# Optimization experiments

Hardware: AMD Instinct MI355X
Metric: run time of the kernel (lower is better)

Reference implementation:

```python
import jax, jax.numpy as jnp
import numpy as np

L, R = -0.1, 1.1          # HardKuma stretched support
MAX_REL = 11              # max relative distance
CLAMP_LO, CLAMP_HI = 0.01, 100.0


def setup_inputs() -> dict:
    key = jax.random.key(0)
    ks = jax.random.split(key, 12)
    B, T, Din, Dout = 4, 2048, 512, 256
    s_in = 0.02
    return {
        "q": jax.random.normal(ks[0], (B, T, Din), jnp.float32),
        "k": jax.random.normal(ks[1], (B, T, Din), jnp.float32),
        "Wa1": jax.random.normal(ks[2], (Din, Dout), jnp.float32) * s_in,
        "ba1": jnp.zeros((Dout,), jnp.float32),
        "Wa2": jax.random.normal(ks[3], (Dout, Dout), jnp.float32) * s_in,
        "ba2": jnp.zeros((Dout,), jnp.float32),
        "Wb1": jax.random.normal(ks[4], (Din, Dout), jnp.float32) * s_in,
        "bb1": jnp.zeros((Dout,), jnp.float32),
        "Wb2": jax.random.normal(ks[5], (Dout, Dout), jnp.float32) * s_in,
        "bb2": jnp.zeros((Dout,), jnp.float32),
        "dist_emb": jax.random.normal(ks[6], (2 * MAX_REL + 1,), jnp.float32) * 0.02,
    }


def _mlp(x, W1, b1, W2, b2):
    # Sequential(Linear, ReLU, Dropout, Linear, ReLU, Dropout) in eval mode
    h = jax.nn.relu(x @ W1 + b1)
    return jax.nn.relu(h @ W2 + b2)


def _rel_dists(T, dist_emb):
    i = jnp.arange(T)
    rel = jnp.clip(i[None, :] - i[:, None], -MAX_REL, MAX_REL) + MAX_REL  # [T,T] ints in [0,22]
    return dist_emb[rel]  # [T,T]


def _kuma_cdf(t, a, b):
    # F(t; a, b) = 1 - (1 - t^a)^b, t is a positive Python-float constant
    return 1.0 - jnp.power(1.0 - jnp.power(t, a), b)


def _kuma_mean(a, b):
    # E[X] = b * Beta(1 + 1/a, b)
    g = 1.0 + 1.0 / a
    return b * jnp.exp(jax.scipy.special.gammaln(g) + jax.scipy.special.gammaln(b)
                       - jax.scipy.special.gammaln(g + b))


def reference(q, k, Wa1, ba1, Wa2, ba2, Wb1, bb1, Wb2, bb2, dist_emb):
    T = q.shape[1]
    q_a = _mlp(q, Wa1, ba1, Wa2, ba2)
    k_a = _mlp(k, Wa1, ba1, Wa2, ba2)
    q_b = _mlp(q, Wb1, bb1, Wb2, bb2)
    k_b = _mlp(k, Wb1, bb1, Wb2, bb2)

    a = jnp.einsum("btd,bsd->bts", q_a, k_a)  # [B,T,T]
    b = jnp.einsum("btd,bsd->bts", q_b, k_b)

    rd = _rel_dists(T, dist_emb)[None]  # [1,T,T]
    a = a + rd
    b = b + rd

    a = jnp.clip(jax.nn.softplus(a), CLAMP_LO, CLAMP_HI)
    b = jnp.clip(jax.nn.softplus(b), CLAMP_LO, CLAMP_HI)

    # HardKuma deterministic (eval) attention
    t0 = (0.0 - L) / (R - L)  # stretched coord of 0
    t1 = (1.0 - L) / (R - L)  # stretched coord of 1
    p0 = _kuma_cdf(t0, a, b)          # P(h = 0)
    p1 = 1.0 - _kuma_cdf(t1, a, b)    # P(h = 1)
    pc = 1.0 - p0 - p1                # continuous mass

    mean = jnp.clip(L + (R - L) * _kuma_mean(a, b), 0.0, 1.0)
    zero_one = jnp.where(p0 > p1, 0.0, 1.0)
    att = jnp.where(pc < 0.5, zero_one, mean)
    return att
```

## Files before the change

### kernel.cpp

```cpp
#include <hip/hip_runtime.h>
#include <hip/hip_bf16.h>
#include <math.h>

typedef __hip_bfloat16 bf16;
typedef short bf16x8 __attribute__((ext_vector_type(8)));
typedef float f32x4 __attribute__((ext_vector_type(4)));
typedef float f32x2 __attribute__((ext_vector_type(2)));

union alignas(16) Pack8 { bf16 h[8]; bf16x8 v; };

#define EXP2F(x) __builtin_amdgcn_exp2f(x)
#define LOG2F(x) __builtin_amdgcn_logf(x)
#define RCPF(x)  __builtin_amdgcn_rcpf(x)

#define TAB_N   64
#define TAB_LO  (-0.35f)
#define TAB_HI  (1.25f)
#define TAB_STRIDE 65

__device__ __forceinline__ float stirl2s(float z) {
    float iz = 1.f / z;
    return (z - 0.5f) * LOG2F(z) - 1.44269504f * z + 1.32574806f
         + iz * (0.12022651f - 0.00400749f * iz * iz);
}
__device__ __forceinline__ float sp4s(float x) {
    return (x * (x + 1.f)) * ((x + 2.f) * (x + 3.f));
}
__device__ float mean_f32(float sa, float sb) {
    float lw = LOG2F(1.f + EXP2F(sa * 1.44269504f));
    float lv = LOG2F(1.f + EXP2F(sb * 1.44269504f));
    lw = fminf(fmaxf(lw, 0.01442695f), 144.269504f);
    lv = fminf(fmaxf(lv, 0.01442695f), 144.269504f);
    float b = 0.69314718f * lv;
    float g = 1.44269504f / lw + 1.f;
    float gb = g + b;
    float lb2 = stirl2s(g + 4.f) + stirl2s(b + 4.f) - stirl2s(gb + 4.f)
              + LOG2F(sp4s(gb) / (sp4s(g) * sp4s(b)));
    float mean = fmaf(1.2f * b, EXP2F(lb2), -0.1f);
    return fminf(fmaxf(mean, 0.f), 1.f);
}

__global__ void prep_weights(const float* __restrict__ Wa1, const float* __restrict__ Wa2,
                             const float* __restrict__ Wb1, const float* __restrict__ Wb2,
                             bf16* __restrict__ oa1, bf16* __restrict__ oa2,
                             bf16* __restrict__ ob1, bf16* __restrict__ ob2,
                             float* __restrict__ tab) {
    if (blockIdx.x >= 1536) {
        int idx = (blockIdx.x - 1536) * 256 + threadIdx.x;
        if (idx >= TAB_N * TAB_N) return;
        int ia = idx >> 6, ib = idx & 63;
        const float step = (TAB_HI - TAB_LO) / (TAB_N - 1);
        float sa  = TAB_LO + ia * step;
        float sb  = TAB_LO + ib * step;
        int ib1 = ib < TAB_N - 1 ? ib + 1 : ib;
        float sb1 = TAB_LO + ib1 * step;
        tab[(ia * TAB_STRIDE + ib) * 2]     = mean_f32(sa, sb);
        tab[(ia * TAB_STRIDE + ib) * 2 + 1] = mean_f32(sa, sb1);
        return;
    }
    int idx = blockIdx.x * 256 + threadIdx.x;
    if (idx < 131072) {
        int n = idx >> 9, k = idx & 511;
        oa1[idx] = __float2bfloat16(Wa1[k * 256 + n]);
    } else if (idx < 196608) {
        int i = idx - 131072; int n = i >> 8, k = i & 255;
        oa2[i] = __float2bfloat16(Wa2[k * 256 + n]);
    } else if (idx < 327680) {
        int i = idx - 196608; int n = i >> 9, k = i & 511;
        ob1[i] = __float2bfloat16(Wb1[k * 256 + n]);
    } else {
        int i = idx - 327680; int n = i >> 8, k = i & 255;
        ob2[i] = __float2bfloat16(Wb2[k * 256 + n]);
    }
}

__global__ __launch_bounds__(512, 4)
void mlp_fused(const float* __restrict__ q, const float* __restrict__ k,
               const bf16* __restrict__ Wa1t, const bf16* __restrict__ Wa2t,
               const bf16* __restrict__ Wb1t, const bf16* __restrict__ Wb2t,
               bf16* __restrict__ qa, bf16* __restrict__ ka,
               bf16* __restrict__ qb, bf16* __restrict__ kb) {
    const int z = blockIdx.z;
    const float* X  = (z & 1) ? k : q;
    const bf16*  W1 = (z >> 1) ? Wb1t : Wa1t;
    const bf16*  W2 = (z >> 1) ? Wb2t : Wa2t;
    bf16* Y = (z == 0) ? qa : (z == 1) ? ka : (z == 2) ? qb : kb;
    const int m0 = blockIdx.x * 64;

    __shared__ alignas(16) char smem[54272];
    short* lB = (short*)smem;
    short* lH = (short*)(smem + 20480);
    short* lA = (short*)(smem + 20480);

    const int tid  = threadIdx.x;
    const int wave = tid >> 6, lane = tid & 63;
    const int wn = wave * 32;
    const int quad = lane >> 4, r16 = lane & 15;

    {
        f32x4 acc[4][2] = {};
        for (int kk = 0; kk < 512; kk += 32) {
            if (tid < 256) {
                int r = tid >> 2, c = (tid & 3) * 8;
                const float* p = X + (size_t)(m0 + r) * 512 + kk + c;
                Pack8 u;
#pragma unroll
                for (int j = 0; j < 8; j++) u.h[j] = __float2bfloat16(p[j]);
                *(bf16x8*)&lA[r * 40 + c] = u.v;
            }
            for (int i = tid; i < 1024; i += 512) {
                int r = i >> 2, c = (i & 3) * 8;
                *(bf16x8*)&lB[r * 40 + c] =
                    *(const bf16x8*)(W1 + (size_t)r * 512 + kk + c);
            }
            __syncthreads();
            bf16x8 af[4], bfr[2];
#pragma unroll
            for (int f = 0; f < 4; f++)
                af[f] = *(const bf16x8*)&lA[(f * 16 + r16) * 40 + quad * 8];
#pragma unroll
            for (int f = 0; f < 2; f++)
                bfr[f] = *(const bf16x8*)&lB[(wn + f * 16 + r16) * 40 + quad * 8];
#pragma unroll
            for (int i = 0; i < 4; i++)
#pragma unroll
                for (int j = 0; j < 2; j++)
                    acc[i][j] = __builtin_amdgcn_mfma_f32_16x16x32_bf16(
                        af[i], bfr[j], acc[i][j], 0, 0, 0);
            __syncthreads();
        }
#pragma unroll
        for (int i = 0; i < 4; i++)
#pragma unroll
            for (int j = 0; j < 2; j++)
#pragma unroll
                for (int r = 0; r < 4; r++) {
                    float v = acc[i][j][r];
                    v = v > 0.f ? v : 0.f;
                    ((bf16*)lH)[(i * 16 + quad * 4 + r) * 264 + wn + j * 16 + r16] =
                        __float2bfloat16(v);
                }
    }
    __syncthreads();

    f32x4 acc2[4][2] = {};
    for (int kk = 0; kk < 256; kk += 32) {
        for (int i = tid; i < 1024; i += 512) {
            int r = i >> 2, c = (i & 3) * 8;
            *(bf16x8*)&lB[r * 40 + c] =
                *(const bf16x8*)(W2 + (size_t)r * 256 + kk + c);
        }
        __syncthreads();
        bf16x8 af[4], bfr[2];
#pragma unroll
        for (int f = 0; f < 4; f++)
            af[f] = *(const bf16x8*)&lH[(f * 16 + r16) * 264 + kk + quad * 8];
#pragma unroll
        for (int f = 0; f < 2; f++)
            bfr[f] = *(const bf16x8*)&lB[(wn + f * 16 + r16) * 40 + quad * 8];
#pragma unroll
        for (int i = 0; i < 4; i++)
#pragma unroll
            for (int j = 0; j < 2; j++)
                acc2[i][j] = __builtin_amdgcn_mfma_f32_16x16x32_bf16(
                    af[i], bfr[j], acc2[i][j], 0, 0, 0);
        __syncthreads();
    }

#pragma unroll
    for (int i = 0; i < 4; i++) {
        int rbase = m0 + i * 16 + quad * 4;
#pragma unroll
        for (int j = 0; j < 2; j++) {
            int col = wn + j * 16 + r16;
#pragma unroll
            for (int r = 0; r < 4; r++) {
                float v = acc2[i][j][r];
                v = v > 0.f ? v : 0.f;
                Y[(size_t)(rbase + r) * 256 + col] = __float2bfloat16(v);
            }
        }
    }
}

__device__ __forceinline__ f32x2 vexp2(f32x2 x) {
    f32x2 r; r.x = EXP2F(x.x); r.y = EXP2F(x.y); return r;
}
__device__ __forceinline__ f32x2 vlog2(f32x2 x) {
    f32x2 r; r.x = LOG2F(x.x); r.y = LOG2F(x.y); return r;
}
__device__ __forceinline__ f32x2 vrcp(f32x2 x) {
    f32x2 r; r.x = RCPF(x.x); r.y = RCPF(x.y); return r;
}
__device__ __forceinline__ f32x2 vclamp(f32x2 x, float lo, float hi) {
    f32x2 r;
    r.x = fminf(fmaxf(x.x, lo), hi);
    r.y = fminf(fmaxf(x.y, lo), hi);
    return r;
}

__device__ __noinline__ f32x2 hardkuma_slow(f32x2 la, f32x2 lb) {
    const float LOG2E = 1.44269504f;
    f32x2 lw = vlog2(1.f + vexp2(la * LOG2E));
    f32x2 lv = vlog2(1.f + vexp2(lb * LOG2E));
    lw = vclamp(lw, 0.01442695f, 144.269504f);
    lv = vclamp(lv, 0.01442695f, 144.269504f);
    f32x2 b = 0.69314718f * lv;

    f32x2 t0a = vexp2(-2.48490665f * lw);
    f32x2 t1a = vexp2(-0.08701138f * lw);
    f32x2 q0 = vexp2(b * vlog2(1.f - t0a));
    f32x2 p1 = vexp2(b * vlog2(1.f - t1a));
    f32x2 pc = q0 - p1;
    f32x2 p0 = 1.f - q0;

    f32x2 g  = 1.44269504f * vrcp(lw) + 1.f;
    f32x2 gb = g + b;
    f32x2 g2 = g + 2.f, b2 = b + 2.f, gb2 = gb + 2.f;

    f32x2 s = (g + 1.5f) * vlog2(g2) + (b + 1.5f) * vlog2(b2)
            - (gb + 1.5f) * vlog2(gb2);

    const float C1 = 0.12022459f;
    const float C2 = -0.00400749f;
    f32x2 pg  = g2 * b2;
    f32x2 rr3 = vrcp(pg * gb2);
    f32x2 ig  = rr3 * (b2 * gb2);
    f32x2 ib  = rr3 * (g2 * gb2);
    f32x2 igb = rr3 * pg;
    f32x2 corr = ig  * (C1 + C2 * (ig  * ig))
               + ib  * (C1 + C2 * (ib  * ib))
               - igb * (C1 + C2 * (igb * igb));
    s += corr - 1.55964202f;

    f32x2 ng = g * (g + 1.f), nb = b * (b + 1.f), ngb = gb * (gb + 1.f);
    s += vlog2(ngb * vrcp(ng * nb));

    f32x2 mean = (1.2f * b) * vexp2(s) - 0.1f;
    mean = vclamp(mean, 0.f, 1.f);

    f32x2 att;
    att.x = (pc.x < 0.5f) ? ((p0.x > p1.x) ? 0.f : 1.f) : mean.x;
    att.y = (pc.y < 0.5f) ? ((p0.y > p1.y) ? 0.f : 1.f) : mean.y;
    return att;
}

__global__ __launch_bounds__(512, 4)
void kuma_attn(const bf16* __restrict__ qa, const bf16* __restrict__ ka,
               const bf16* __restrict__ qb, const bf16* __restrict__ kb,
               const float* __restrict__ dist_emb, const float* __restrict__ tabg,
               float* __restrict__ out) {
    const int bidx = blockIdx.z;
    const int t0 = blockIdx.x * 128;
    const int s0 = blockIdx.y * 128;

    __shared__ alignas(16) char smem[41052];
    short* lQa = (short*)smem;
    short* lQb = (short*)(smem + 10240);
    short* lKa = (short*)(smem + 20480);
    short* lKb = (short*)(smem + 30720);
    float* sTab  = (float*)smem;
    float* sDist = (float*)(smem + 40960);

    const int tid = threadIdx.x;
    if (tid < 23) sDist[tid] = dist_emb[tid];

    const int wave = tid >> 6, lane = tid & 63;
    const int wm = (wave >> 2) * 64;
    const int wn = (wave & 3) * 32;
    const int quad = lane >> 4, r16 = lane & 15;
    const size_t base = (size_t)bidx * 2048 * 256;

    f32x4 accA[4][2] = {};
    f32x4 accB[4][2] = {};

    const int r0 = tid >> 2, c0 = (tid & 3) * 8;

    for (int kk = 0; kk < 256; kk += 32) {
        {
            size_t gq = base + (size_t)(t0 + r0) * 256 + kk + c0;
            size_t gk = base + (size_t)(s0 + r0) * 256 + kk + c0;
            *(bf16x8*)&lQa[r0 * 40 + c0] = *(const bf16x8*)(qa + gq);
            *(bf16x8*)&lQb[r0 * 40 + c0] = *(const bf16x8*)(qb + gq);
            *(bf16x8*)&lKa[r0 * 40 + c0] = *(const bf16x8*)(ka + gk);
            *(bf16x8*)&lKb[r0 * 40 + c0] = *(const bf16x8*)(kb + gk);
        }
        __syncthreads();
        bf16x8 aA[4], aB[4], bA[2], bB[2];
#pragma unroll
        for (int f = 0; f < 4; f++) {
            int ar = (wm + f * 16 + r16) * 40 + quad * 8;
            aA[f] = *(const bf16x8*)&lQa[ar];
            aB[f] = *(const bf16x8*)&lQb[ar];
        }
#pragma unroll
        for (int f = 0; f < 2; f++) {
            int br = (wn + f * 16 + r16) * 40 + quad * 8;
            bA[f] = *(const bf16x8*)&lKa[br];
            bB[f] = *(const bf16x8*)&lKb[br];
        }
#pragma unroll
        for (int i = 0; i < 4; i++)
#pragma unroll
            for (int j = 0; j < 2; j++) {
                accA[i][j] = __builtin_amdgcn_mfma_f32_16x16x32_bf16(
                    aA[i], bA[j], accA[i][j], 0, 0, 0);
                accB[i][j] = __builtin_amdgcn_mfma_f32_16x16x32_bf16(
                    aB[i], bB[j], accB[i][j], 0, 0, 0);
            }
        __syncthreads();
    }

    for (int i = tid; i < (TAB_N * TAB_STRIDE * 2) / 4; i += 512)
        ((f32x4*)sTab)[i] = ((const f32x4*)tabg)[i];
    __syncthreads();

    const float SCALE = (TAB_N - 1) / (TAB_HI - TAB_LO);
#pragma unroll
    for (int i = 0; i < 4; i++) {
#pragma unroll
        for (int j = 0; j < 2; j++) {
            int s = s0 + wn + j * 16 + r16;
#pragma unroll
            for (int rr = 0; rr < 2; rr++) {
                int t = t0 + wm + i * 16 + quad * 4 + rr * 2;
                int d0 = s - t;
                int d1 = d0 - 1;
                d0 = d0 < -11 ? -11 : (d0 > 11 ? 11 : d0);
                d1 = d1 < -11 ? -11 : (d1 > 11 ? 11 : d1);
                float rd0 = sDist[d0 + 11];
                float rd1 = sDist[d1 + 11];
                f32x2 la  = { accA[i][j][rr * 2] + rd0, accA[i][j][rr * 2 + 1] + rd1 };
                f32x2 lbv = { accB[i][j][rr * 2] + rd0, accB[i][j][rr * 2 + 1] + rd1 };

                float mn = fminf(fminf(la.x, la.y), fminf(lbv.x, lbv.y));
                float mx = fmaxf(fmaxf(la.x, la.y), fmaxf(lbv.x, lbv.y));

                f32x2 u = vclamp((la  - TAB_LO) * SCALE, 0.f, (float)(TAB_N - 1));
                f32x2 v = vclamp((lbv - TAB_LO) * SCALE, 0.f, (float)(TAB_N - 1));
                int ia0 = (int)u.x; ia0 = ia0 > TAB_N - 2 ? TAB_N - 2 : ia0;
                int ia1 = (int)u.y; ia1 = ia1 > TAB_N - 2 ? TAB_N - 2 : ia1;
                int ib0 = (int)v.x; ib0 = ib0 > TAB_N - 2 ? TAB_N - 2 : ib0;
                int ib1 = (int)v.y; ib1 = ib1 > TAB_N - 2 ? TAB_N - 2 : ib1;
                f32x2 fa = { u.x - (float)ia0, u.y - (float)ia1 };
                f32x2 fb = { v.x - (float)ib0, v.y - (float)ib1 };
                int o0 = (ia0 * TAB_STRIDE + ib0) * 2;
                int o1 = (ia1 * TAB_STRIDE + ib1) * 2;
                f32x2 e0r0 = *(const f32x2*)&sTab[o0];
                f32x2 e0r1 = *(const f32x2*)&sTab[o0 + TAB_STRIDE * 2];
                f32x2 e1r0 = *(const f32x2*)&sTab[o1];
                f32x2 e1r1 = *(const f32x2*)&sTab[o1 + TAB_STRIDE * 2];
                f32x2 m0 = { e0r0.x + fb.x * (e0r0.y - e0r0.x),
                             e1r0.x + fb.y * (e1r0.y - e1r0.x) };
                f32x2 m1 = { e0r1.x + fb.x * (e0r1.y - e0r1.x),
                             e1r1.x + fb.y * (e1r1.y - e1r1.x) };
                f32x2 att = m0 + fa * (m1 - m0);

                bool oob = (mn < TAB_LO) | (mx > TAB_HI);
                if (__builtin_expect(__any(oob), 0)) {
                    f32x2 ex = hardkuma_slow(la, lbv);
                    if (oob) att = ex;
                }

                out[((size_t)bidx * 2048 + t) * 2048 + s] = att.x;
                out[((size_t)bidx * 2048 + t + 1) * 2048 + s] = att.y;
            }
        }
    }
}

extern "C" void kernel_launch(void* const* d_in, const int* in_sizes, int n_in,
                              void* d_out, int out_size, void* d_ws, size_t ws_size,
                              hipStream_t stream) {
    const float* q    = (const float*)d_in[0];
    const float* k    = (const float*)d_in[1];
    const float* Wa1  = (const float*)d_in[2];
    const float* Wa2  = (const float*)d_in[4];
    const float* Wb1  = (const float*)d_in[6];
    const float* Wb2  = (const float*)d_in[8];
    const float* dist = (const float*)d_in[10];
    float* out = (float*)d_out;

    bf16* wsbf = (bf16*)d_ws;
    bf16* Wa1t = wsbf;
    bf16* Wa2t = Wa1t + 131072;
    bf16* Wb1t = Wa2t + 65536;
    bf16* Wb2t = Wb1t + 131072;
    bf16* qa   = Wb2t + 65536;
    bf16* ka   = qa + 2097152;
    bf16* qb   = ka + 2097152;
    bf16* kb   = qb + 2097152;
    bf16* tail = kb + 2097152;
    float* tabg = (float*)tail;

    prep_weights<<<1552, 256, 0, stream>>>(Wa1, Wa2, Wb1, Wb2,
                                           Wa1t, Wa2t, Wb1t, Wb2t, tabg);

    dim3 g1(128, 1, 4), blk512(512, 1, 1);
    mlp_fused<<<g1, blk512, 0, stream>>>(q, k, Wa1t, Wa2t, Wb1t, Wb2t,
                                         qa, ka, qb, kb);

    dim3 g2(16, 16, 4);
    kuma_attn<<<g2, blk512, 0, stream>>>(qa, ka, qb, kb, dist, tabg, out);
}
```

Measured before the change: 185.9 us.

## Use direct global-to-LDS loads and widen K tile to 64 in both GEMM kernels

Replaces register-staged global-to-shared copies of weights and Q/K projections with global_load_lds 16-byte direct loads, and doubles the K step per iteration from 32 to 64, which halves the number of barriers. The goal is to cut VGPR traffic and synchronisation overhead in the MLP and attention GEMM phases. The shared layouts lose their padding (row stride 64 instead of 40), which risks LDS bank conflicts on the MFMA fragment reads. LDS use per block also grows (up to about 66 KB), which may lower occupancy.

```diff
diff --git a/kernel.cpp b/kernel.cpp
--- a/kernel.cpp
+++ b/kernel.cpp
@@ -12,6 +12,12 @@
 #define EXP2F(x) __builtin_amdgcn_exp2f(x)
 #define LOG2F(x) __builtin_amdgcn_logf(x)
 #define RCPF(x)  __builtin_amdgcn_rcpf(x)
+
+__device__ __forceinline__ void gload16(const void* g, void* l) {
+    __builtin_amdgcn_global_load_lds(
+        (const __attribute__((address_space(1))) void*)g,
+        (__attribute__((address_space(3))) void*)l, 16, 0, 0);
+}
 
 #define TAB_N   64
 #define TAB_LO  (-0.35f)
@@ -87,46 +93,52 @@
     bf16* Y = (z == 0) ? qa : (z == 1) ? ka : (z == 2) ? qb : kb;
     const int m0 = blockIdx.x * 64;
 
-    __shared__ alignas(16) char smem[54272];
+    __shared__ alignas(16) char smem[66560];
     short* lB = (short*)smem;
-    short* lH = (short*)(smem + 20480);
-    short* lA = (short*)(smem + 20480);
+    short* lH = (short*)(smem + 32768);
+    short* lA = (short*)(smem + 32768);
 
     const int tid  = threadIdx.x;
     const int wave = tid >> 6, lane = tid & 63;
     const int wn = wave * 32;
     const int quad = lane >> 4, r16 = lane & 15;
+    const int srow = lane >> 3, scol = (lane & 7) * 8;
+    const int car = tid >> 3,  cac = (tid & 7) * 8;
 
     {
         f32x4 acc[4][2] = {};
-        for (int kk = 0; kk < 512; kk += 32) {
-            if (tid < 256) {
-                int r = tid >> 2, c = (tid & 3) * 8;
-                const float* p = X + (size_t)(m0 + r) * 512 + kk + c;
+        for (int kk = 0; kk < 512; kk += 64) {
+            {
+                const float* p = X + (size_t)(m0 + car) * 512 + kk + cac;
                 Pack8 u;
 #pragma unroll
                 for (int j = 0; j < 8; j++) u.h[j] = __float2bfloat16(p[j]);
-                *(bf16x8*)&lA[r * 40 + c] = u.v;
-            }
-            for (int i = tid; i < 1024; i += 512) {
-                int r = i >> 2, c = (i & 3) * 8;
-                *(bf16x8*)&lB[r * 40 + c] =
-                    *(const bf16x8*)(W1 + (size_t)r * 512 + kk + c);
+                *(bf16x8*)&lA[car * 64 + cac] = u.v;
+            }
+#pragma unroll
+            for (int j = 0; j < 4; j++) {
+                int row = wave * 32 + j * 8 + srow;
+                gload16(W1 + (size_t)row * 512 + kk + scol,
+                        lB + (wave * 32 + j * 8) * 64);
             }
             __syncthreads();
-            bf16x8 af[4], bfr[2];
-#pragma unroll
-            for (int f = 0; f < 4; f++)
-                af[f] = *(const bf16x8*)&lA[(f * 16 + r16) * 40 + quad * 8];
-#pragma unroll
-            for (int f = 0; f < 2; f++)
-                bfr[f] = *(const bf16x8*)&lB[(wn + f * 16 + r16) * 40 + quad * 8];
-#pragma unroll
-            for (int i = 0; i < 4; i++)
-#pragma unroll
-                for (int j = 0; j < 2; j++)
-                    acc[i][j] = __builtin_amdgcn_mfma_f32_16x16x32_bf16(
-                        af[i], bfr[j], acc[i][j], 0, 0, 0);
+#pragma unroll
+            for (int ks = 0; ks < 2; ks++) {
+                int co = ks * 32 + quad * 8;
+                bf16x8 af[4], bfr[2];
+#pragma unroll
+                for (int f = 0; f < 4; f++)
+                    af[f] = *(const bf16x8*)&lA[(f * 16 + r16) * 64 + co];
+#pragma unroll
+                for (int f = 0; f < 2; f++)
+                    bfr[f] = *(const bf16x8*)&lB[(wn + f * 16 + r16) * 64 + co];
+#pragma unroll
+                for (int i = 0; i < 4; i++)
+#pragma unroll
+                    for (int j = 0; j < 2; j++)
+                        acc[i][j] = __builtin_amdgcn_mfma_f32_16x16x32_bf16(
+                            af[i], bfr[j], acc[i][j], 0, 0, 0);
+            }
             __syncthreads();
         }
 #pragma unroll
@@ -144,26 +156,31 @@
     __syncthreads();
 
     f32x4 acc2[4][2] = {};
-    for (int kk = 0; kk < 256; kk += 32) {
-        for (int i = tid; i < 1024; i += 512) {
-            int r = i >> 2, c = (i & 3) * 8;
-            *(bf16x8*)&lB[r * 40 + c] =
-                *(const bf16x8*)(W2 + (size_t)r * 256 + kk + c);
+    for (int kk = 0; kk < 256; kk += 64) {
+#pragma unroll
+        for (int j = 0; j < 4; j++) {
+            int row = wave * 32 + j * 8 + srow;
+            gload16(W2 + (size_t)row * 256 + kk + scol,
+                    lB + (wave * 32 + j * 8) * 64);
         }
         __syncthreads();
-        bf16x8 af[4], bfr[2];
-#pragma unroll
-        for (int f = 0; f < 4; f++)
-            af[f] = *(const bf16x8*)&lH[(f * 16 + r16) * 264 + kk + quad * 8];
-#pragma unroll
-        for (int f = 0; f < 2; f++)
-            bfr[f] = *(const bf16x8*)&lB[(wn + f * 16 + r16) * 40 + quad * 8];
-#pragma unroll
-        for (int i = 0; i < 4; i++)
-#pragma unroll
-            for (int j = 0; j < 2; j++)
-                acc2[i][j] = __builtin_amdgcn_mfma_f32_16x16x32_bf16(
-                    af[i], bfr[j], acc2[i][j], 0, 0, 0);
+#pragma unroll
+        for (int ks = 0; ks < 2; ks++) {
+            int co = kk + ks * 32 + quad * 8;
+            bf16x8 af[4], bfr[2];
+#pragma unroll
+            for (int f = 0; f < 4; f++)
+                af[f] = *(const bf16x8*)&lH[(f * 16 + r16) * 264 + co];
+#pragma unroll
+            for (int f = 0; f < 2; f++)
+                bfr[f] = *(const bf16x8*)&lB[(wn + f * 16 + r16) * 64 + ks * 32 + quad * 8];
+#pragma unroll
+            for (int i = 0; i < 4; i++)
+#pragma unroll
+                for (int j = 0; j < 2; j++)
+                    acc2[i][j] = __builtin_amdgcn_mfma_f32_16x16x32_bf16(
+                        af[i], bfr[j], acc2[i][j], 0, 0, 0);
+        }
         __syncthreads();
     }
 
@@ -254,13 +271,13 @@
     const int t0 = blockIdx.x * 128;
     const int s0 = blockIdx.y * 128;
 
-    __shared__ alignas(16) char smem[41052];
+    __shared__ alignas(16) char smem[65628];
     short* lQa = (short*)smem;
-    short* lQb = (short*)(smem + 10240);
-    short* lKa = (short*)(smem + 20480);
-    short* lKb = (short*)(smem + 30720);
+    short* lQb = (short*)(smem + 16384);
+    short* lKa = (short*)(smem + 32768);
+    short* lKb = (short*)(smem + 49152);
     float* sTab  = (float*)smem;
-    float* sDist = (float*)(smem + 40960);
+    float* sDist = (float*)(smem + 65536);
 
     const int tid = threadIdx.x;
     if (tid < 23) sDist[tid] = dist_emb[tid];
@@ -271,43 +288,50 @@
     const int quad = lane >> 4, r16 = lane & 15;
     const size_t base = (size_t)bidx * 2048 * 256;
 
+    const int srow = lane >> 3, scol = (lane & 7) * 8;
+
     f32x4 accA[4][2] = {};
     f32x4 accB[4][2] = {};
 
-    const int r0 = tid >> 2, c0 = (tid & 3) * 8;
-
-    for (int kk = 0; kk < 256; kk += 32) {
-        {
-            size_t gq = base + (size_t)(t0 + r0) * 256 + kk + c0;
-            size_t gk = base + (size_t)(s0 + r0) * 256 + kk + c0;
-            *(bf16x8*)&lQa[r0 * 40 + c0] = *(const bf16x8*)(qa + gq);
-            *(bf16x8*)&lQb[r0 * 40 + c0] = *(const bf16x8*)(qb + gq);
-            *(bf16x8*)&lKa[r0 * 40 + c0] = *(const bf16x8*)(ka + gk);
-            *(bf16x8*)&lKb[r0 * 40 + c0] = *(const bf16x8*)(kb + gk);
+    for (int kk = 0; kk < 256; kk += 64) {
+#pragma unroll
+        for (int j = 0; j < 2; j++) {
+            int row = wave * 16 + j * 8 + srow;
+            size_t gq = base + (size_t)(t0 + row) * 256 + kk + scol;
+            size_t gk = base + (size_t)(s0 + row) * 256 + kk + scol;
+            int ld = (wave * 16 + j * 8) * 64;
+            gload16(qa + gq, lQa + ld);
+            gload16(qb + gq, lQb + ld);
+            gload16(ka + gk, lKa + ld);
+            gload16(kb + gk, lKb + ld);
         }
         __syncthreads();
-        bf16x8 aA[4], aB[4], bA[2], bB[2];
-#pragma unroll
-        for (int f = 0; f < 4; f++) {
-            int ar = (wm + f * 16 + r16) * 40 + quad * 8;
-            aA[f] = *(const bf16x8*)&lQa[ar];
-            aB[f] = *(const bf16x8*)&lQb[ar];
-        }
-#pragma unroll
-        for (int f = 0; f < 2; f++) {
-            int br = (wn + f * 16 + r16) * 40 + quad * 8;
-            bA[f] = *(const bf16x8*)&lKa[br];
-            bB[f] = *(const bf16x8*)&lKb[br];
-        }
-#pragma unroll
-        for (int i = 0; i < 4; i++)
-#pragma unroll
-            for (int j = 0; j < 2; j++) {
-                accA[i][j] = __builtin_amdgcn_mfma_f32_16x16x32_bf16(
-                    aA[i], bA[j], accA[i][j], 0, 0, 0);
-                accB[i][j] = __builtin_amdgcn_mfma_f32_16x16x32_bf16(
-                    aB[i], bB[j], accB[i][j], 0, 0, 0);
-            }
+#pragma unroll
+        for (int ks = 0; ks < 2; ks++) {
+            int co = ks * 32 + quad * 8;
+            bf16x8 aA[4], aB[4], bA[2], bB[2];
+#pragma unroll
+            for (int f = 0; f < 4; f++) {
+                int ar = (wm + f * 16 + r16) * 64 + co;
+                aA[f] = *(const bf16x8*)&lQa[ar];
+                aB[f] = *(const bf16x8*)&lQb[ar];
+            }
+#pragma unroll
+            for (int f = 0; f < 2; f++) {
+                int br = (wn + f * 16 + r16) * 64 + co;
+                bA[f] = *(const bf16x8*)&lKa[br];
+                bB[f] = *(const bf16x8*)&lKb[br];
+            }
+#pragma unroll
+            for (int i = 0; i < 4; i++)
+#pragma unroll
+                for (int j = 0; j < 2; j++) {
+                    accA[i][j] = __builtin_amdgcn_mfma_f32_16x16x32_bf16(
+                        aA[i], bA[j], accA[i][j], 0, 0, 0);
+                    accB[i][j] = __builtin_amdgcn_mfma_f32_16x16x32_bf16(
+                        aB[i], bB[j], accB[i][j], 0, 0, 0);
+                }
+        }
         __syncthreads();
     }
 
```

After: 180.7 us. 2.8% less time.
